# Kernel tuning notes

Hardware: AMD Instinct MI355X
Metric: run time of the kernel (lower is better)

The kernel has to match this reference:

```python
import jax, jax.numpy as jnp
import numpy as np

N, K_IN, K_OUT = 200000, 8, 4
E, D, H, O = 800000, 64, 128, 1


def setup_inputs() -> dict:
    key = jax.random.key(0)
    ks = jax.random.split(key, 8)
    edges = jax.random.normal(ks[0], (E, D), dtype=jnp.float32)
    in_idx = jax.random.randint(ks[1], (N, K_IN), 0, E, dtype=jnp.int32)
    in_mask = jax.random.randint(ks[2], (N, K_IN), 0, 2, dtype=jnp.int32)
    out_idx = jax.random.randint(ks[3], (N, K_OUT), 0, E, dtype=jnp.int32)
    out_mask = jax.random.randint(ks[4], (N, K_OUT), 0, 2, dtype=jnp.int32)
    # FC stack params: layer0 takes 2*D (edge feat ++ pooled attention context)
    W0 = jax.random.normal(ks[5], (H, 2 * D), dtype=jnp.float32) * (1.0 / np.sqrt(2 * D))
    b0 = jnp.zeros((H,), dtype=jnp.float32)
    W1 = jax.random.normal(ks[6], (H, H), dtype=jnp.float32) * (1.0 / np.sqrt(H))
    b1 = jnp.zeros((H,), dtype=jnp.float32)
    Wout = jax.random.normal(ks[7], (O, H), dtype=jnp.float32) * (1.0 / np.sqrt(H))
    bout = jnp.zeros((O,), dtype=jnp.float32)
    return {"edges": edges, "in_idx": in_idx, "in_mask": in_mask,
            "out_idx": out_idx, "out_mask": out_mask,
            "W0": W0, "b0": b0, "W1": W1, "b1": b1, "Wout": Wout, "bout": bout}


def _forward(edges, in_idx, in_mask, out_idx, out_mask, W0, b0, W1, b1, Wout, bout):
    d = edges.shape[1]
    mbool = in_mask.astype(bool)                       # [N, K_in]
    mf = in_mask.astype(edges.dtype)[..., None]        # [N, K_in, 1]
    # gather per-node in-edge sets: [N, K_in, D]
    Ein = edges[in_idx]
    # self-attention over the in-edge set (query=key=value=in_edges)
    scores = jnp.einsum('nqd,nkd->nqk', Ein, Ein) / jnp.sqrt(jnp.asarray(d, edges.dtype))
    scores = jnp.where(mbool[:, None, :], scores, jnp.asarray(-1e9, edges.dtype))
    attn = jax.nn.softmax(scores, axis=-1)
    att_out = jnp.einsum('nqk,nkd->nqd', attn, Ein)    # [N, K_in, D]
    # pool attended rows over valid queries -> weighted_in_edges [N, D]
    denom = jnp.maximum(mf.sum(axis=1), 1.0)
    pooled = (att_out * mf).sum(axis=1) / denom
    # per out-edge: concat(edge_feat, pooled) -> MLP
    Eout = edges[out_idx]                              # [N, K_out, D]
    pooled_b = jnp.broadcast_to(pooled[:, None, :], Eout.shape)
    x = jnp.concatenate([Eout, pooled_b], axis=-1)     # [N, K_out, 2D]
    h = jax.nn.relu(jnp.einsum('nkd,hd->nkh', x, W0) + b0)
    h = jax.nn.relu(jnp.einsum('nkh,gh->nkg', h, W1) + b1)
    y = jnp.einsum('nkh,oh->nko', h, Wout) + bout      # [N, K_out, O]
    y = y * out_mask.astype(y.dtype)[..., None]        # zero padded out-edges
    return y.reshape(-1, y.shape[-1])                  # [N*K_out, O]


def reference(edges, in_idx, in_mask, out_idx, out_mask, W0, b0, W1, b1, Wout, bout):
    return _forward(edges, in_idx, in_mask, out_idx, out_mask, W0, b0, W1, b1, Wout, bout)
```

## Files before the change

### kernel.cpp

```cpp
#include <hip/hip_runtime.h>
#include <math.h>

#define D 64
#define H 128
#define KIN 8
#define KOUT 4
#define ELD16 72
#define XLDB 136
#define BROWS 128

typedef __attribute__((ext_vector_type(8))) short short8v;
typedef __attribute__((ext_vector_type(4))) float f32x4;

__device__ inline unsigned short f2bf(float f) {
    union { float f; unsigned u; } v; v.f = f;
    unsigned r = v.u + 0x7FFF + ((v.u >> 16) & 1);
    return (unsigned short)(r >> 16);
}

__global__ void convert_w_kernel(const float* __restrict__ W0,
                                 const float* __restrict__ W1,
                                 unsigned short* __restrict__ Wbf) {
    const int i = blockIdx.x * 256 + threadIdx.x;
    const float v = (i < H*H) ? W0[i] : W1[i - H*H];
    Wbf[i] = f2bf(v);
}

__global__ __launch_bounds__(256, 6) void attn_kernel(
    const float* __restrict__ edges,
    const int*   __restrict__ in_idx,
    const int*   __restrict__ in_mask,
    unsigned short* __restrict__ pooled,
    int nodeBase, int nodeEnd)
{
    __shared__ __align__(16) unsigned short eins[4][16][ELD16];
    const int tid  = threadIdx.x;
    const int wave = tid >> 6;
    const int lane = tid & 63;
    const int col  = lane & 15;
    const int grp  = lane >> 4;
    const int n0   = nodeBase + blockIdx.x * 8 + wave * 2;
    if (n0 >= nodeEnd) return;

    const int   idx_l = in_idx [(size_t)n0*KIN + col];
    const float mkcol = (float)in_mask[(size_t)n0*KIN + col];

    float ein_r[16];
    #pragma unroll
    for (int r = 0; r < 16; ++r)
        ein_r[r] = edges[(size_t)__shfl(idx_l, r) * D + lane];
    #pragma unroll
    for (int r = 0; r < 16; ++r) eins[wave][r][lane] = f2bf(ein_r[r]);

    const short8v f0 = *(const short8v*)&eins[wave][col][grp*8];
    const short8v f1 = *(const short8v*)&eins[wave][col][32 + grp*8];
    f32x4 sc = (f32x4){0.f, 0.f, 0.f, 0.f};
    sc = __builtin_amdgcn_mfma_f32_16x16x32_bf16(f0, f0, sc, 0, 0, 0);
    sc = __builtin_amdgcn_mfma_f32_16x16x32_bf16(f1, f1, sc, 0, 0, 0);

    float s0, s1, s2, s3;
    {
        const bool kv = (mkcol > 0.f);
        #define MSK(jj, sv) { const int row = grp*4 + jj; \
            const bool ok = kv && ((row < 8) == (col < 8)); \
            sv = ok ? sc[jj] * 0.125f : -1e9f; }
        MSK(0, s0) MSK(1, s1) MSK(2, s2) MSK(3, s3)
        #undef MSK
    }
    float m0=s0, m1=s1, m2=s2, m3=s3;
    #pragma unroll
    for (int off = 1; off < 16; off <<= 1) {
        m0 = fmaxf(m0, __shfl_xor(m0, off));
        m1 = fmaxf(m1, __shfl_xor(m1, off));
        m2 = fmaxf(m2, __shfl_xor(m2, off));
        m3 = fmaxf(m3, __shfl_xor(m3, off));
    }
    float e0=__expf(s0-m0), e1=__expf(s1-m1), e2=__expf(s2-m2), e3=__expf(s3-m3);
    float t0=e0, t1=e1, t2=e2, t3=e3;
    #pragma unroll
    for (int off = 1; off < 16; off <<= 1) {
        t0 += __shfl_xor(t0, off); t1 += __shfl_xor(t1, off);
        t2 += __shfl_xor(t2, off); t3 += __shfl_xor(t3, off);
    }
    float wsum = __shfl(mkcol, grp*4 + 0) * (e0 / t0)
               + __shfl(mkcol, grp*4 + 1) * (e1 / t1)
               + __shfl(mkcol, grp*4 + 2) * (e2 / t2)
               + __shfl(mkcol, grp*4 + 3) * (e3 / t3);
    wsum += __shfl_xor(wsum, 16);
    wsum += __shfl_xor(wsum, 32);

    float dn = mkcol;
    dn += __shfl_xor(dn, 1); dn += __shfl_xor(dn, 2); dn += __shfl_xor(dn, 4);
    const float dnA = fmaxf(__shfl(dn, 0), 1.f);
    const float dnB = fmaxf(__shfl(dn, 8), 1.f);

    float pA = 0.f, pB = 0.f;
    #pragma unroll
    for (int k = 0; k < 8; ++k) {
        pA += __shfl(wsum, k)     * ein_r[k];
        pB += __shfl(wsum, 8 + k) * ein_r[8 + k];
    }
    const size_t pbase = (size_t)(n0 - nodeBase) * D;
    pooled[pbase + lane]     = f2bf(pA / dnA);
    pooled[pbase + D + lane] = f2bf(pB / dnB);
}

__global__ __launch_bounds__(256, 4) void mlp_kernel(
    const float* __restrict__ edges,
    const int*   __restrict__ out_idx,
    const int*   __restrict__ out_mask,
    const float* __restrict__ b0, const float* __restrict__ b1,
    const float* __restrict__ Wout, const float* __restrict__ bout,
    const unsigned short* __restrict__ Wbf,
    const unsigned short* __restrict__ pooled,
    float* __restrict__ out,
    int nodeBase, int nodeEnd)
{
    __shared__ __align__(16) unsigned short xbuf[BROWS][XLDB];
    const int tid  = threadIdx.x;
    const int wave = tid >> 6;
    const int lane = tid & 63;
    const int rowBase = (nodeBase + blockIdx.x * 32) * KOUT;
    const int rowEnd  = nodeEnd * KOUT;

    #pragma unroll 4
    for (int rr = 0; rr < 32; ++rr) {
        const int row  = wave * 32 + rr;
        const int grow = rowBase + row;
        if (grow < rowEnd) {
            const int n  = grow >> 2;
            const int oi = out_idx[grow];
            xbuf[row][lane]     = f2bf(edges[(size_t)oi * D + lane]);
            xbuf[row][D + lane] = pooled[(size_t)(n - nodeBase) * D + lane];
        }
    }
    __syncthreads();

    const int l15  = lane & 15;
    const int kofs = (lane >> 4) * 8;
    const int rrow = (lane >> 4) * 4;
    const int rowb = (wave >> 1) * 64;
    const int colb = (wave & 1) * 64;

    #pragma unroll
    for (int layer = 0; layer < 2; ++layer) {
        const unsigned short* __restrict__ Wl = Wbf + layer * (H*H);
        const float* __restrict__ bl = layer ? b1 : b0;

        f32x4 acc[4][4];
        #pragma unroll
        for (int ct = 0; ct < 4; ++ct) {
            const float bv = bl[colb + ct*16 + l15];
            #pragma unroll
            for (int rt = 0; rt < 4; ++rt) acc[rt][ct] = (f32x4){bv, bv, bv, bv};
        }
        #pragma unroll
        for (int ks = 0; ks < 4; ++ks) {
            short8v bfr[4];
            #pragma unroll
            for (int ct = 0; ct < 4; ++ct)
                bfr[ct] = *(const short8v*)&Wl[(size_t)(colb + ct*16 + l15) * H + ks*32 + kofs];
            #pragma unroll
            for (int rt = 0; rt < 4; ++rt) {
                const short8v a = *(const short8v*)&xbuf[rowb + rt*16 + l15][ks*32 + kofs];
                #pragma unroll
                for (int ct = 0; ct < 4; ++ct)
                    acc[rt][ct] = __builtin_amdgcn_mfma_f32_16x16x32_bf16(a, bfr[ct], acc[rt][ct], 0, 0, 0);
            }
        }
        __syncthreads();
        #pragma unroll
        for (int rt = 0; rt < 4; ++rt)
            #pragma unroll
            for (int ct = 0; ct < 4; ++ct)
                #pragma unroll
                for (int j = 0; j < 4; ++j)
                    xbuf[rowb + rt*16 + rrow + j][colb + ct*16 + l15] =
                        f2bf(fmaxf(acc[rt][ct][j], 0.f));
        __syncthreads();
    }

    {
        const int row = tid >> 1;
        const int kh  = tid & 1;
        float p = 0.f;
        #pragma unroll
        for (int m = 0; m < 8; ++m) {
            const int k0 = kh*64 + m*8;
            const short8v hv = *(const short8v*)&xbuf[row][k0];
            const float4 w0 = *(const float4*)&Wout[k0];
            const float4 w1 = *(const float4*)&Wout[k0 + 4];
            union { unsigned u; float f; } c;
            c.u = ((unsigned)(unsigned short)hv[0]) << 16; p += c.f * w0.x;
            c.u = ((unsigned)(unsigned short)hv[1]) << 16; p += c.f * w0.y;
            c.u = ((unsigned)(unsigned short)hv[2]) << 16; p += c.f * w0.z;
            c.u = ((unsigned)(unsigned short)hv[3]) << 16; p += c.f * w0.w;
            c.u = ((unsigned)(unsigned short)hv[4]) << 16; p += c.f * w1.x;
            c.u = ((unsigned)(unsigned short)hv[5]) << 16; p += c.f * w1.y;
            c.u = ((unsigned)(unsigned short)hv[6]) << 16; p += c.f * w1.z;
            c.u = ((unsigned)(unsigned short)hv[7]) << 16; p += c.f * w1.w;
        }
        p += __shfl_xor(p, 1);
        const int grow = rowBase + row;
        if (kh == 0 && grow < rowEnd)
            out[grow] = (p + bout[0]) * (float)out_mask[grow];
    }
}

extern "C" void kernel_launch(void* const* d_in, const int* in_sizes, int n_in,
                              void* d_out, int out_size, void* d_ws, size_t ws_size,
                              hipStream_t stream)
{
    const float* edges  = (const float*)d_in[0];
    const int* in_idx   = (const int*)d_in[1];
    const int* in_mask  = (const int*)d_in[2];
    const int* out_idx  = (const int*)d_in[3];
    const int* out_mask = (const int*)d_in[4];
    const float* W0   = (const float*)d_in[5];
    const float* b0   = (const float*)d_in[6];
    const float* W1   = (const float*)d_in[7];
    const float* b1   = (const float*)d_in[8];
    const float* Wout = (const float*)d_in[9];
    const float* bout = (const float*)d_in[10];
    float* out = (float*)d_out;

    unsigned short* Wbf       = (unsigned short*)d_ws;
    unsigned short* pooledBuf = (unsigned short*)((char*)d_ws + 65536);

    const int nNodes = in_sizes[1] / KIN;
    convert_w_kernel<<<(2*H*H + 255) / 256, 256, 0, stream>>>(W0, W1, Wbf);

    const size_t avail = (ws_size > 65536) ? ws_size - 65536 : 0;
    long long maxNodes = (long long)(avail / (D * sizeof(unsigned short)));
    int chunk = (int)((maxNodes / 32) * 32);
    if (chunk <= 0) chunk = 32;
    if (chunk > nNodes) chunk = nNodes;

    for (int base = 0; base < nNodes; base += chunk) {
        const int end = (base + chunk < nNodes) ? base + chunk : nNodes;
        const int cn  = end - base;
        attn_kernel<<<(cn + 7) / 8, 256, 0, stream>>>(
            edges, in_idx, in_mask, pooledBuf, base, end);
        mlp_kernel<<<(cn + 31) / 32, 256, 0, stream>>>(
            edges, out_idx, out_mask, b0, b1, Wout, bout,
            Wbf, pooledBuf, out, base, end);
    }
}
```

Baseline: 588.0 us.

## Make MLP kernel persistent with register-resident weights and double-buffered gathers

The MLP kernel becomes a persistent grid of fixed size that loops over 64-row chunks. Each wave keeps its 32-column slice of W0 and W1 in registers, and the gather of the next chunk's edge and pooled rows is issued before the current chunk's MFMAs, then written into a second shared buffer. The final output projection is fused into the layer-1 epilogue through shuffle reductions and a small shared partial-sum array. This is meant to hide gather latency and avoid reloading weights per block, at the cost of higher register pressure (launch bounds lowered to 3 waves per SIMD) and a fixed grid size.

Result: slower. 647.1 us (+10.1%).

```diff
diff --git a/kernel.cpp b/kernel.cpp
--- a/kernel.cpp
+++ b/kernel.cpp
@@ -7,7 +7,8 @@
 #define KOUT 4
 #define ELD16 72
 #define XLDB 136
-#define BROWS 128
+#define CHROWS 64
+#define MLPGRID 768
 
 typedef __attribute__((ext_vector_type(8))) short short8v;
 typedef __attribute__((ext_vector_type(4))) float f32x4;
@@ -105,7 +106,7 @@
     pooled[pbase + D + lane] = f2bf(pB / dnB);
 }
 
-__global__ __launch_bounds__(256, 4) void mlp_kernel(
+__global__ __launch_bounds__(256, 3) void mlp_kernel(
     const float* __restrict__ edges,
     const int*   __restrict__ out_idx,
     const int*   __restrict__ out_mask,
@@ -116,95 +117,147 @@
     float* __restrict__ out,
     int nodeBase, int nodeEnd)
 {
-    __shared__ __align__(16) unsigned short xbuf[BROWS][XLDB];
+    __shared__ __align__(16) unsigned short xbuf[2][CHROWS][XLDB];
+    __shared__ __align__(16) unsigned short h0buf[CHROWS][XLDB];
+    __shared__ float ypart[4][CHROWS];
+
     const int tid  = threadIdx.x;
     const int wave = tid >> 6;
     const int lane = tid & 63;
-    const int rowBase = (nodeBase + blockIdx.x * 32) * KOUT;
-    const int rowEnd  = nodeEnd * KOUT;
-
-    #pragma unroll 4
-    for (int rr = 0; rr < 32; ++rr) {
-        const int row  = wave * 32 + rr;
-        const int grow = rowBase + row;
-        if (grow < rowEnd) {
-            const int n  = grow >> 2;
-            const int oi = out_idx[grow];
-            xbuf[row][lane]     = f2bf(edges[(size_t)oi * D + lane]);
-            xbuf[row][D + lane] = pooled[(size_t)(n - nodeBase) * D + lane];
-        }
-    }
+    const int l15  = lane & 15;
+    const int grp  = lane >> 4;
+    const int kofs = grp * 8;
+    const int colb = wave * 32;
+
+    const int rowBeg = nodeBase * KOUT;
+    const int rowEnd = nodeEnd * KOUT;
+    const int nch = (rowEnd - rowBeg + CHROWS - 1) / CHROWS;
+
+    short8v w0[2][4], w1[2][4];
+    #pragma unroll
+    for (int ct = 0; ct < 2; ++ct)
+        #pragma unroll
+        for (int ks = 0; ks < 4; ++ks) {
+            w0[ct][ks] = *(const short8v*)&Wbf[(size_t)(colb + ct*16 + l15)*H + ks*32 + kofs];
+            w1[ct][ks] = *(const short8v*)&Wbf[(size_t)H*H + (size_t)(colb + ct*16 + l15)*H + ks*32 + kofs];
+        }
+    const float bias0[2] = { b0[colb + l15], b0[colb + 16 + l15] };
+    const float bias1[2] = { b1[colb + l15], b1[colb + 16 + l15] };
+    const float wo[2]    = { Wout[colb + l15], Wout[colb + 16 + l15] };
+    const float bo = bout[0];
+
+    float ev[16];
+    unsigned short pv[16];
+
+    #define ISSUE(cc) do { \
+        const int crb_ = rowBeg + (cc) * CHROWS; \
+        _Pragma("unroll") \
+        for (int rr = 0; rr < 16; ++rr) { \
+            const int grow_ = crb_ + wave*16 + rr; \
+            int oi_ = 0, nd_ = nodeBase; \
+            if (grow_ < rowEnd) { oi_ = out_idx[grow_]; nd_ = grow_ >> 2; } \
+            ev[rr] = edges[(size_t)oi_ * D + lane]; \
+            pv[rr] = pooled[(size_t)(nd_ - nodeBase) * D + lane]; \
+        } } while (0)
+    #define WRITE(buf_) do { \
+        _Pragma("unroll") \
+        for (int rr = 0; rr < 16; ++rr) { \
+            const int row_ = wave*16 + rr; \
+            xbuf[buf_][row_][lane]     = f2bf(ev[rr]); \
+            xbuf[buf_][row_][D + lane] = pv[rr]; \
+        } } while (0)
+
+    int c   = blockIdx.x;
+    int cur = 0;
+    if (c < nch) { ISSUE(c); WRITE(0); }
     __syncthreads();
 
-    const int l15  = lane & 15;
-    const int kofs = (lane >> 4) * 8;
-    const int rrow = (lane >> 4) * 4;
-    const int rowb = (wave >> 1) * 64;
-    const int colb = (wave & 1) * 64;
-
-    #pragma unroll
-    for (int layer = 0; layer < 2; ++layer) {
-        const unsigned short* __restrict__ Wl = Wbf + layer * (H*H);
-        const float* __restrict__ bl = layer ? b1 : b0;
-
-        f32x4 acc[4][4];
-        #pragma unroll
-        for (int ct = 0; ct < 4; ++ct) {
-            const float bv = bl[colb + ct*16 + l15];
-            #pragma unroll
-            for (int rt = 0; rt < 4; ++rt) acc[rt][ct] = (f32x4){bv, bv, bv, bv};
-        }
+    for (; c < nch; c += gridDim.x) {
+        const int crb   = rowBeg + c * CHROWS;
+        const int cnext = c + gridDim.x;
+
+        if (cnext < nch) ISSUE(cnext);
+
+        f32x4 acc[4][2];
+        #pragma unroll
+        for (int rt = 0; rt < 4; ++rt)
+            #pragma unroll
+            for (int ct = 0; ct < 2; ++ct) {
+                const float bv = bias0[ct];
+                acc[rt][ct] = (f32x4){bv, bv, bv, bv};
+            }
         #pragma unroll
         for (int ks = 0; ks < 4; ++ks) {
-            short8v bfr[4];
-            #pragma unroll
-            for (int ct = 0; ct < 4; ++ct)
-                bfr[ct] = *(const short8v*)&Wl[(size_t)(colb + ct*16 + l15) * H + ks*32 + kofs];
-            #pragma unroll
-            for (int rt = 0; rt < 4; ++rt) {
-                const short8v a = *(const short8v*)&xbuf[rowb + rt*16 + l15][ks*32 + kofs];
+            short8v a[4];
+            #pragma unroll
+            for (int rt = 0; rt < 4; ++rt)
+                a[rt] = *(const short8v*)&xbuf[cur][rt*16 + l15][ks*32 + kofs];
+            #pragma unroll
+            for (int rt = 0; rt < 4; ++rt)
                 #pragma unroll
-                for (int ct = 0; ct < 4; ++ct)
-                    acc[rt][ct] = __builtin_amdgcn_mfma_f32_16x16x32_bf16(a, bfr[ct], acc[rt][ct], 0, 0, 0);
-            }
-        }
-        __syncthreads();
+                for (int ct = 0; ct < 2; ++ct)
+                    acc[rt][ct] = __builtin_amdgcn_mfma_f32_16x16x32_bf16(a[rt], w0[ct][ks], acc[rt][ct], 0, 0, 0);
+        }
+
         #pragma unroll
         for (int rt = 0; rt < 4; ++rt)
             #pragma unroll
-            for (int ct = 0; ct < 4; ++ct)
+            for (int ct = 0; ct < 2; ++ct)
                 #pragma unroll
                 for (int j = 0; j < 4; ++j)
-                    xbuf[rowb + rt*16 + rrow + j][colb + ct*16 + l15] =
+                    h0buf[rt*16 + grp*4 + j][colb + ct*16 + l15] =
                         f2bf(fmaxf(acc[rt][ct][j], 0.f));
         __syncthreads();
-    }
-
-    {
-        const int row = tid >> 1;
-        const int kh  = tid & 1;
-        float p = 0.f;
-        #pragma unroll
-        for (int m = 0; m < 8; ++m) {
-            const int k0 = kh*64 + m*8;
-            const short8v hv = *(const short8v*)&xbuf[row][k0];
-            const float4 w0 = *(const float4*)&Wout[k0];
-            const float4 w1 = *(const float4*)&Wout[k0 + 4];
-            union { unsigned u; float f; } c;
-            c.u = ((unsigned)(unsigned short)hv[0]) << 16; p += c.f * w0.x;
-            c.u = ((unsigned)(unsigned short)hv[1]) << 16; p += c.f * w0.y;
-            c.u = ((unsigned)(unsigned short)hv[2]) << 16; p += c.f * w0.z;
-            c.u = ((unsigned)(unsigned short)hv[3]) << 16; p += c.f * w0.w;
-            c.u = ((unsigned)(unsigned short)hv[4]) << 16; p += c.f * w1.x;
-            c.u = ((unsigned)(unsigned short)hv[5]) << 16; p += c.f * w1.y;
-            c.u = ((unsigned)(unsigned short)hv[6]) << 16; p += c.f * w1.z;
-            c.u = ((unsigned)(unsigned short)hv[7]) << 16; p += c.f * w1.w;
-        }
-        p += __shfl_xor(p, 1);
-        const int grow = rowBase + row;
-        if (kh == 0 && grow < rowEnd)
-            out[grow] = (p + bout[0]) * (float)out_mask[grow];
-    }
+
+        #pragma unroll
+        for (int rt = 0; rt < 4; ++rt)
+            #pragma unroll
+            for (int ct = 0; ct < 2; ++ct) {
+                const float bv = bias1[ct];
+                acc[rt][ct] = (f32x4){bv, bv, bv, bv};
+            }
+        #pragma unroll
+        for (int ks = 0; ks < 4; ++ks) {
+            short8v a[4];
+            #pragma unroll
+            for (int rt = 0; rt < 4; ++rt)
+                a[rt] = *(const short8v*)&h0buf[rt*16 + l15][ks*32 + kofs];
+            #pragma unroll
+            for (int rt = 0; rt < 4; ++rt)
+                #pragma unroll
+                for (int ct = 0; ct < 2; ++ct)
+                    acc[rt][ct] = __builtin_amdgcn_mfma_f32_16x16x32_bf16(a[rt], w1[ct][ks], acc[rt][ct], 0, 0, 0);
+        }
+
+        #pragma unroll
+        for (int rt = 0; rt < 4; ++rt) {
+            #pragma unroll
+            for (int j = 0; j < 4; ++j) {
+                float p = fmaxf(acc[rt][0][j], 0.f) * wo[0]
+                        + fmaxf(acc[rt][1][j], 0.f) * wo[1];
+                p += __shfl_xor(p, 1);
+                p += __shfl_xor(p, 2);
+                p += __shfl_xor(p, 4);
+                p += __shfl_xor(p, 8);
+                if (l15 == 0) ypart[wave][rt*16 + grp*4 + j] = p;
+            }
+        }
+        __syncthreads();
+        if (tid < CHROWS) {
+            const int grow = crb + tid;
+            if (grow < rowEnd) {
+                const float y = ypart[0][tid] + ypart[1][tid]
+                              + ypart[2][tid] + ypart[3][tid] + bo;
+                out[grow] = y * (float)out_mask[grow];
+            }
+        }
+
+        if (cnext < nch) WRITE(cur ^ 1);
+        __syncthreads();
+        cur ^= 1;
+    }
+    #undef ISSUE
+    #undef WRITE
 }
 
 extern "C" void kernel_launch(void* const* d_in, const int* in_sizes, int n_in,
@@ -241,7 +294,7 @@
         const int cn  = end - base;
         attn_kernel<<<(cn + 7) / 8, 256, 0, stream>>>(
             edges, in_idx, in_mask, pooledBuf, base, end);
-        mlp_kernel<<<(cn + 31) / 32, 256, 0, stream>>>(
+        mlp_kernel<<<MLPGRID, 256, 0, stream>>>(
             edges, out_idx, out_mask, b0, b1, Wout, bout,
             Wbf, pooledBuf, out, base, end);
     }
```
